# Kernel tuning notes

Measured on AMD Instinct MI355X. Metric: run time of the kernel, lower is better.

Reference implementation:

```python
import jax, jax.numpy as jnp
import numpy as np

N = 10000      # nodes
E = 160000     # edges
D = 512        # hidden = input channels (residual requires equality)
OUT = 128      # output channels
G = 64         # graphs in batch


def setup_inputs() -> dict:
    key = jax.random.key(0)
    ks = jax.random.split(key, 16)
    s = 1.0 / np.sqrt(D)
    inp = {
        "x": jax.random.normal(ks[0], (N, D), jnp.float32) * 0.1,
        "edge_index": jax.random.randint(ks[1], (2, E), 0, N, dtype=jnp.int64),
        "batch": jnp.sort(jax.random.randint(ks[2], (N,), 0, G, dtype=jnp.int64)),
    }
    for i in range(5):
        inp[f"Wr{i+1}"] = jax.random.uniform(ks[3 + 2 * i], (D, D), jnp.float32, -s, s)  # lin_rel weight
        inp[f"Ws{i+1}"] = jax.random.uniform(ks[4 + 2 * i], (D, D), jnp.float32, -s, s)  # lin_root weight (no bias)
        inp[f"b{i+1}"] = jnp.zeros((D,), jnp.float32)                                     # lin_rel bias
    inp["Wlin"] = jax.random.uniform(ks[13], (D, OUT), jnp.float32, -s, s)
    inp["blin"] = jnp.zeros((OUT,), jnp.float32)
    return inp


def graph_conv(x, src, dst, Wr, Ws, b):
    # PyG GraphConv(aggr='add'): out = lin_rel(sum_{j in N(i)} x_j) + lin_root(x_i)
    agg = jax.ops.segment_sum(x[src], dst, num_segments=N)  # [N, D] scatter-add
    return agg @ Wr + b + x @ Ws


def reference(x, Wr1, Ws1, b1, Wr2, Ws2, b2, Wr3, Ws3, b3, Wr4, Ws4, b4, Wr5, Ws5, b5, Wlin, blin, edge_index, batch):
    src, dst = edge_index[0], edge_index[1]
    x = jax.nn.relu(x + graph_conv(x, src, dst, Wr1, Ws1, b1))
    x = jax.nn.relu(x + graph_conv(x, src, dst, Wr2, Ws2, b2))
    x = jax.nn.relu(x + graph_conv(x, src, dst, Wr3, Ws3, b3))
    x = jax.nn.relu(x + graph_conv(x, src, dst, Wr4, Ws4, b4))
    x = x + graph_conv(x, src, dst, Wr5, Ws5, b5)  # no relu after conv5
    # global_mean_pool over graph ids
    sums = jax.ops.segment_sum(x, batch, num_segments=G)                       # [G, D]
    cnt = jax.ops.segment_sum(jnp.ones((N, 1), x.dtype), batch, num_segments=G)
    x = sums / jnp.maximum(cnt, 1.0)
    return x @ Wlin + blin  # [G, OUT]
```

## Files before the change

### kernel.cpp

```cpp
#include <hip/hip_runtime.h>
#include <hip/hip_bf16.h>

#define NN 10000
#define EE 160000
#define DD 512
#define GG 64
#define OUTC 128
#define NBLK 628

typedef __attribute__((ext_vector_type(8))) short bf16x8;
typedef __attribute__((ext_vector_type(4))) float f32x4;

static __device__ __forceinline__ unsigned short f2bf(float f) {
  unsigned u = __builtin_bit_cast(unsigned, f);
  unsigned rounding = 0x7fffu + ((u >> 16) & 1u);
  u += rounding;
  return (unsigned short)(u >> 16);
}

static __device__ __forceinline__ void gload_lds16(const void* g, void* l) {
  __builtin_amdgcn_global_load_lds(
      (const __attribute__((address_space(1))) unsigned*)g,
      (__attribute__((address_space(3))) unsigned*)l, 16, 0, 0);
}

struct WPtrs { const float* p[10]; };

__global__ __launch_bounds__(256) void prep_all(
    WPtrs wp, unsigned short* __restrict__ WT,
    const float* __restrict__ x_in, unsigned short* __restrict__ m0,
    const int* __restrict__ batch, int* __restrict__ gstart,
    const int* __restrict__ dstv, int* __restrict__ deg) {
  int bid = blockIdx.x;
  int tid = threadIdx.x;
  if (bid < 2560) {
    __shared__ float tile[32][33];
    int z = bid >> 8;
    int rem = bid & 255;
    int by = (rem >> 4) * 32, bx = (rem & 15) * 32;
    const float* W = wp.p[z];
    unsigned short* dst = WT + (size_t)(z >> 1) * DD * 1024 + (size_t)(z & 1) * DD;
    int tx = tid & 31, ty = tid >> 5;
    for (int i = ty; i < 32; i += 8)
      tile[i][tx] = W[(size_t)(by + i) * DD + bx + tx];
    __syncthreads();
    int addI = z & 1;
    for (int i = ty; i < 32; i += 8) {
      float v = tile[tx][i];
      if (addI && (by + tx) == (bx + i)) v += 1.0f;
      dst[(size_t)(bx + i) * 1024 + by + tx] = f2bf(v);
    }
  } else if (bid < 12560) {
    int i = (bid - 2560) * 256 + tid;
    if (i < NN * DD / 2) {
      float2 v = ((const float2*)x_in)[i];
      unsigned u = (unsigned)f2bf(v.x) | ((unsigned)f2bf(v.y) << 16);
      int e = i << 1;
      int row = e >> 9, col = e & 511;
      ((unsigned*)m0)[row * 512 + 256 + (col >> 1)] = u;
    }
  } else if (bid < 12600) {
    int i = (bid - 12560) * 256 + tid;
    if (i < NN) {
      int cur = batch[i];
      int prev = (i == 0) ? -1 : batch[i - 1];
      for (int g = prev + 1; g <= cur; ++g) gstart[g] = i;
      if (i == NN - 1)
        for (int g = cur + 1; g <= GG; ++g) gstart[g] = NN;
    }
  } else {
    int e = (bid - 12600) * 256 + tid;
    if (e < EE) atomicAdd(&deg[dstv[e]], 1);
  }
}

__global__ void scan_offsets(const int* __restrict__ cnt, int* __restrict__ offs) {
  __shared__ int wpre[17];
  __shared__ int carry;
  int t = threadIdx.x;
  int lane = t & 63, wv = t >> 6;
  if (t == 0) carry = 0;
  __syncthreads();
  for (int base = 0; base < NN; base += 1024) {
    int i = base + t;
    int v = (i < NN) ? cnt[i] : 0;
    int s = v;
#pragma unroll
    for (int d = 1; d < 64; d <<= 1) {
      int o = __shfl_up(s, d, 64);
      if (lane >= d) s += o;
    }
    if (lane == 63) wpre[wv] = s;
    __syncthreads();
    if (t == 0) {
      int r = 0;
      for (int w = 0; w < 16; ++w) { int x = wpre[w]; wpre[w] = r; r += x; }
      wpre[16] = r;
    }
    __syncthreads();
    int incl = s + wpre[wv] + carry;
    if (i < NN) offs[i] = incl - v;
    __syncthreads();
    if (t == 0) carry += wpre[16];
    __syncthreads();
  }
  if (t == 0) offs[NN] = carry;
}

__global__ void fill_edges(const int* __restrict__ src, const int* __restrict__ dst,
                           const int* __restrict__ offs, int* __restrict__ fptr,
                           int* __restrict__ ssrc) {
  int e = blockIdx.x * 256 + threadIdx.x;
  if (e < EE) {
    int d = dst[e];
    int p = atomicAdd(&fptr[d], 1);
    ssrc[offs[d] + p] = src[e];
  }
}

__global__ __launch_bounds__(256) void seg_sum2(unsigned short* __restrict__ merged,
                                                const int* __restrict__ offs,
                                                const int* __restrict__ ssrc) {
  int bid = blockIdx.x;
  int slice = bid & 3;
  int p = bid >> 2;
  int wave = threadIdx.x >> 6, lane = threadIdx.x & 63;
  int na = p * 4 + wave;
  int nb = na + 5000;
  const unsigned* xw = (const unsigned*)merged;
  size_t co = 256 + slice * 64 + lane;
  int e0 = offs[na], f0 = offs[na + 1];
  int e1 = offs[nb], f1 = offs[nb + 1];
  float a0 = 0.f, a1 = 0.f, b0 = 0.f, b1 = 0.f;
#define LD(n, ee, i) unsigned n = xw[(size_t)ssrc[(ee) + (i)] * 512 + co]
#define AC(n, x0, x1)                                   \
  x0 += __builtin_bit_cast(float, n << 16);             \
  x1 += __builtin_bit_cast(float, n & 0xffff0000u)
  while (e0 + 8 <= f0 && e1 + 8 <= f1) {
    LD(u0, e0, 0); LD(u1, e0, 1); LD(u2, e0, 2); LD(u3, e0, 3);
    LD(u4, e0, 4); LD(u5, e0, 5); LD(u6, e0, 6); LD(u7, e0, 7);
    LD(w0, e1, 0); LD(w1, e1, 1); LD(w2, e1, 2); LD(w3, e1, 3);
    LD(w4, e1, 4); LD(w5, e1, 5); LD(w6, e1, 6); LD(w7, e1, 7);
    AC(u0, a0, a1); AC(u1, a0, a1); AC(u2, a0, a1); AC(u3, a0, a1);
    AC(u4, a0, a1); AC(u5, a0, a1); AC(u6, a0, a1); AC(u7, a0, a1);
    AC(w0, b0, b1); AC(w1, b0, b1); AC(w2, b0, b1); AC(w3, b0, b1);
    AC(w4, b0, b1); AC(w5, b0, b1); AC(w6, b0, b1); AC(w7, b0, b1);
    e0 += 8; e1 += 8;
  }
  for (; e0 + 4 <= f0; e0 += 4) {
    LD(u0, e0, 0); LD(u1, e0, 1); LD(u2, e0, 2); LD(u3, e0, 3);
    AC(u0, a0, a1); AC(u1, a0, a1); AC(u2, a0, a1); AC(u3, a0, a1);
  }
  for (; e0 < f0; ++e0) {
    LD(u0, e0, 0); AC(u0, a0, a1);
  }
  for (; e1 + 4 <= f1; e1 += 4) {
    LD(w0, e1, 0); LD(w1, e1, 1); LD(w2, e1, 2); LD(w3, e1, 3);
    AC(w0, b0, b1); AC(w1, b0, b1); AC(w2, b0, b1); AC(w3, b0, b1);
  }
  for (; e1 < f1; ++e1) {
    LD(w0, e1, 0); AC(w0, b0, b1);
  }
#undef LD
#undef AC
  unsigned oa = (unsigned)f2bf(a0) | ((unsigned)f2bf(a1) << 16);
  unsigned ob = (unsigned)f2bf(b0) | ((unsigned)f2bf(b1) << 16);
  ((unsigned*)merged)[(size_t)na * 512 + slice * 64 + lane] = oa;
  ((unsigned*)merged)[(size_t)nb * 512 + slice * 64 + lane] = ob;
}

__global__ __launch_bounds__(256) void gemm_layer(
    const unsigned short* __restrict__ Am,
    const unsigned short* __restrict__ Bw,
    const float* __restrict__ bias,
    unsigned short* __restrict__ xout,
    int do_relu) {
  __shared__ unsigned short Al[2][64 * 64];
  __shared__ unsigned short Bl[2][128 * 64];
  int tid = threadIdx.x;
  int lane = tid & 63, wave = tid >> 6;
  int wr = wave >> 1, wc = wave & 1;

  int orig = blockIdx.x;
  int xcd = orig & 7, cidx = orig >> 3;
  int wgid = (xcd < 4) ? xcd * 79 + cidx : 316 + (xcd - 4) * 78 + cidx;
  int brow = (wgid >> 2) * 64;
  int bcol = (wgid & 3) * 128;
  int lrow = lane & 15, lq = lane >> 4;

  f32x4 acc[2][4];
#pragma unroll
  for (int m = 0; m < 2; ++m)
#pragma unroll
    for (int n = 0; n < 4; ++n) acc[m][n] = (f32x4){0.f, 0.f, 0.f, 0.f};

  auto STAGE = [&](int buf, int t) {
    int k0 = t * 64;
#pragma unroll
    for (int i = 0; i < 2; ++i) {
      int idx = i * 256 + tid;
      int row = idx >> 3, c = idx & 7;
      int csw = (c ^ (row & 7)) * 8;
      int gr = brow + row;
      if (gr >= NN) gr = NN - 1;
      gload_lds16(Am + (size_t)gr * 1024 + k0 + csw, &Al[buf][idx * 8]);
    }
#pragma unroll
    for (int i = 0; i < 4; ++i) {
      int idx = i * 256 + tid;
      int row = idx >> 3, c = idx & 7;
      int csw = (c ^ (row & 7)) * 8;
      gload_lds16(Bw + (size_t)(bcol + row) * 1024 + k0 + csw, &Bl[buf][idx * 8]);
    }
  };

  STAGE(0, 0);
  __syncthreads();
  int cur = 0;
#pragma unroll 1
  for (int t = 0; t < 16; ++t) {
    if (t < 15) STAGE(cur ^ 1, t + 1);
#pragma unroll
    for (int kk = 0; kk < 2; ++kk) {
      bf16x8 a[2], b[4];
      int lc = kk * 4 + lq;
#pragma unroll
      for (int m = 0; m < 2; ++m) {
        int row = wr * 32 + m * 16 + lrow;
        a[m] = *(const bf16x8*)&Al[cur][row * 64 + ((lc ^ (lrow & 7)) * 8)];
      }
#pragma unroll
      for (int n = 0; n < 4; ++n) {
        int row = wc * 64 + n * 16 + lrow;
        b[n] = *(const bf16x8*)&Bl[cur][row * 64 + ((lc ^ (lrow & 7)) * 8)];
      }
#pragma unroll
      for (int m = 0; m < 2; ++m)
#pragma unroll
        for (int n = 0; n < 4; ++n)
          acc[m][n] = __builtin_amdgcn_mfma_f32_16x16x32_bf16(a[m], b[n], acc[m][n], 0, 0, 0);
    }
    __syncthreads();
    cur ^= 1;
  }

  int crow = lq * 4, ccol = lrow;
#pragma unroll
  for (int m = 0; m < 2; ++m) {
#pragma unroll
    for (int n = 0; n < 4; ++n) {
      int col = bcol + wc * 64 + n * 16 + ccol;
      float bv = bias[col];
#pragma unroll
      for (int i = 0; i < 4; ++i) {
        int row = brow + wr * 32 + m * 16 + crow + i;
        if (row < NN) {
          float v = acc[m][n][i] + bv;
          if (do_relu) v = fmaxf(v, 0.f);
          xout[(size_t)row * 1024 + 512 + col] = f2bf(v);
        }
      }
    }
  }
}

__global__ __launch_bounds__(256) void pool_partial(const unsigned short* __restrict__ mfin,
                                                    const int* __restrict__ gstart,
                                                    float* __restrict__ pooled) {
  int g = blockIdx.x, part = blockIdx.y;
  int t = threadIdx.x;
  int beg = gstart[g], end = gstart[g + 1];
  int n = end - beg;
  int per = (n + 7) >> 3;
  int b = beg + part * per;
  int e = b + per; if (e > end) e = end;
  if (b >= e) return;
  const unsigned* mw = (const unsigned*)mfin;
  float a0 = 0.f, a1 = 0.f;
  for (int r = b; r < e; ++r) {
    unsigned v = mw[(size_t)r * 512 + 256 + t];
    a0 += __builtin_bit_cast(float, v << 16);
    a1 += __builtin_bit_cast(float, v & 0xffff0000u);
  }
  atomicAdd(&pooled[g * DD + 2 * t], a0);
  atomicAdd(&pooled[g * DD + 2 * t + 1], a1);
}

__global__ __launch_bounds__(128) void final_linear(const float* __restrict__ pooled,
                                                    const int* __restrict__ gstart,
                                                    const float* __restrict__ Wlin,
                                                    const float* __restrict__ blin,
                                                    float* __restrict__ out) {
  __shared__ float p[128];
  int g = blockIdx.x, kq = blockIdx.y;
  int o = threadIdx.x;
  int cnt = gstart[g + 1] - gstart[g];
  float inv = 1.0f / fmaxf((float)cnt, 1.0f);
  p[o] = pooled[g * DD + kq * 128 + o] * inv;
  __syncthreads();
  float s = (kq == 0) ? blin[o] : 0.f;
#pragma unroll 8
  for (int k = 0; k < 128; ++k)
    s += p[k] * Wlin[(size_t)(kq * 128 + k) * OUTC + o];
  atomicAdd(&out[g * OUTC + o], s);
}

extern "C" void kernel_launch(void* const* d_in, const int* in_sizes, int n_in,
                              void* d_out, int out_size, void* d_ws, size_t ws_size,
                              hipStream_t stream) {
  const float* x_in = (const float*)d_in[0];
  const int* ei = (const int*)d_in[1];
  const int* src = ei;
  const int* dst = ei + EE;
  const int* batch = (const int*)d_in[2];
  WPtrs wp;
  const float* bias[5];
  for (int l = 0; l < 5; ++l) {
    wp.p[2 * l] = (const float*)d_in[3 + 3 * l];
    wp.p[2 * l + 1] = (const float*)d_in[4 + 3 * l];
    bias[l] = (const float*)d_in[5 + 3 * l];
  }
  const float* Wlin = (const float*)d_in[18];
  const float* blin = (const float*)d_in[19];
  float* out = (float*)d_out;

  char* ws = (char*)d_ws;
  size_t off = 0;
  auto alloc = [&](size_t bytes) { size_t o = off; off += (bytes + 511) & ~(size_t)511; return o; };
  unsigned short* m0 = (unsigned short*)(ws + alloc((size_t)NN * 1024 * 2));
  unsigned short* m1 = (unsigned short*)(ws + alloc((size_t)NN * 1024 * 2));
  unsigned short* wt = (unsigned short*)(ws + alloc((size_t)5 * DD * 1024 * 2));
  int* deg = (int*)(ws + alloc((size_t)2 * NN * 4));
  int* fptr = deg + NN;
  int* offs = (int*)(ws + alloc((size_t)(NN + 1) * 4));
  int* ssrc = (int*)(ws + alloc((size_t)EE * 4));
  int* gstart = (int*)(ws + alloc((size_t)(GG + 1) * 4));
  float* pooled = (float*)(ws + alloc((size_t)GG * DD * 4));

  hipMemsetAsync(deg, 0, (size_t)2 * NN * 4, stream);
  hipMemsetAsync(pooled, 0, (size_t)GG * DD * 4, stream);
  hipMemsetAsync(out, 0, (size_t)GG * OUTC * 4, stream);

  prep_all<<<13225, 256, 0, stream>>>(wp, wt, x_in, m0, batch, gstart, dst, deg);

  scan_offsets<<<1, 1024, 0, stream>>>(deg, offs);
  fill_edges<<<(EE + 255) / 256, 256, 0, stream>>>(src, dst, offs, fptr, ssrc);

  unsigned short* mc = m0;
  unsigned short* mn = m1;
  for (int l = 0; l < 5; ++l) {
    seg_sum2<<<5000, 256, 0, stream>>>(mc, offs, ssrc);
    gemm_layer<<<NBLK, 256, 0, stream>>>(mc, wt + (size_t)l * DD * 1024,
                                         bias[l], mn, l < 4 ? 1 : 0);
    unsigned short* t = mc; mc = mn; mn = t;
  }

  dim3 pgrid(GG, 8);
  pool_partial<<<pgrid, 256, 0, stream>>>(mc, gstart, pooled);
  dim3 fgrid(GG, 4);
  final_linear<<<fgrid, 128, 0, stream>>>(pooled, gstart, Wlin, blin, out);
}
```

Baseline: 258.9 us.

## Steal segment-sum work per XCD and fuse pooling with final linear

The segment-sum kernel now has each block claim its work item from per-slice atomic counters, choosing first the slice that matches its XCD id. The aim is for the same XCD to keep gathering the same 64-column feature slice so it stays in that XCD's L2. Separately, pool_partial and final_linear are merged into one kernel per graph that computes the mean, does the 512x128 matvec, and writes the output directly. This removes the pooled buffer, two memsets and the float atomics. The cost is one atomic per block and less parallelism in the pooling step (64 blocks instead of 512).

```diff
diff --git a/kernel.cpp b/kernel.cpp
--- a/kernel.cpp
+++ b/kernel.cpp
@@ -118,13 +118,29 @@
   }
 }
 
-__global__ __launch_bounds__(256) void seg_sum2(unsigned short* __restrict__ merged,
-                                                const int* __restrict__ offs,
-                                                const int* __restrict__ ssrc) {
-  int bid = blockIdx.x;
-  int slice = bid & 3;
-  int p = bid >> 2;
-  int wave = threadIdx.x >> 6, lane = threadIdx.x & 63;
+__global__ __launch_bounds__(256) void seg_steal(unsigned short* __restrict__ merged,
+                                                 const int* __restrict__ offs,
+                                                 const int* __restrict__ ssrc,
+                                                 int* __restrict__ ctr) {
+  __shared__ int sel;
+  int tid = threadIdx.x;
+  if (tid == 0) {
+    unsigned xcd = __builtin_amdgcn_s_getreg(20 | (31 << 11));
+    int item = -1;
+#pragma unroll
+    for (int k = 0; k < 4; ++k) {
+      if (item < 0) {
+        int s = (int)((xcd + k) & 3u);
+        int g = atomicAdd(&ctr[s], 1);
+        if (g < 1250) item = s * 1250 + g;
+      }
+    }
+    sel = item;
+  }
+  __syncthreads();
+  int slice = sel / 1250;
+  int p = sel - slice * 1250;
+  int wave = tid >> 6, lane = tid & 63;
   int na = p * 4 + wave;
   int nb = na + 5000;
   const unsigned* xw = (const unsigned*)merged;
@@ -264,45 +280,51 @@
   }
 }
 
-__global__ __launch_bounds__(256) void pool_partial(const unsigned short* __restrict__ mfin,
-                                                    const int* __restrict__ gstart,
-                                                    float* __restrict__ pooled) {
-  int g = blockIdx.x, part = blockIdx.y;
+__global__ __launch_bounds__(256) void pool_final(const unsigned short* __restrict__ mfin,
+                                                  const int* __restrict__ gstart,
+                                                  const float* __restrict__ Wlin,
+                                                  const float* __restrict__ blin,
+                                                  float* __restrict__ out) {
+  __shared__ float pl[DD];
+  __shared__ float red[OUTC];
+  int g = blockIdx.x;
   int t = threadIdx.x;
   int beg = gstart[g], end = gstart[g + 1];
-  int n = end - beg;
-  int per = (n + 7) >> 3;
-  int b = beg + part * per;
-  int e = b + per; if (e > end) e = end;
-  if (b >= e) return;
   const unsigned* mw = (const unsigned*)mfin;
   float a0 = 0.f, a1 = 0.f;
-  for (int r = b; r < e; ++r) {
+  int r = beg;
+  for (; r + 4 <= end; r += 4) {
+    unsigned v0 = mw[(size_t)r * 512 + 256 + t];
+    unsigned v1 = mw[(size_t)(r + 1) * 512 + 256 + t];
+    unsigned v2 = mw[(size_t)(r + 2) * 512 + 256 + t];
+    unsigned v3 = mw[(size_t)(r + 3) * 512 + 256 + t];
+    a0 += __builtin_bit_cast(float, v0 << 16);
+    a1 += __builtin_bit_cast(float, v0 & 0xffff0000u);
+    a0 += __builtin_bit_cast(float, v1 << 16);
+    a1 += __builtin_bit_cast(float, v1 & 0xffff0000u);
+    a0 += __builtin_bit_cast(float, v2 << 16);
+    a1 += __builtin_bit_cast(float, v2 & 0xffff0000u);
+    a0 += __builtin_bit_cast(float, v3 << 16);
+    a1 += __builtin_bit_cast(float, v3 & 0xffff0000u);
+  }
+  for (; r < end; ++r) {
     unsigned v = mw[(size_t)r * 512 + 256 + t];
     a0 += __builtin_bit_cast(float, v << 16);
     a1 += __builtin_bit_cast(float, v & 0xffff0000u);
   }
-  atomicAdd(&pooled[g * DD + 2 * t], a0);
-  atomicAdd(&pooled[g * DD + 2 * t + 1], a1);
-}
-
-__global__ __launch_bounds__(128) void final_linear(const float* __restrict__ pooled,
-                                                    const int* __restrict__ gstart,
-                                                    const float* __restrict__ Wlin,
-                                                    const float* __restrict__ blin,
-                                                    float* __restrict__ out) {
-  __shared__ float p[128];
-  int g = blockIdx.x, kq = blockIdx.y;
-  int o = threadIdx.x;
-  int cnt = gstart[g + 1] - gstart[g];
-  float inv = 1.0f / fmaxf((float)cnt, 1.0f);
-  p[o] = pooled[g * DD + kq * 128 + o] * inv;
-  __syncthreads();
-  float s = (kq == 0) ? blin[o] : 0.f;
+  float inv = 1.0f / fmaxf((float)(end - beg), 1.0f);
+  pl[2 * t] = a0 * inv;
+  pl[2 * t + 1] = a1 * inv;
+  __syncthreads();
+  int o = t & 127, h = t >> 7;
+  float s = 0.f;
+  int kb = h * 256;
 #pragma unroll 8
-  for (int k = 0; k < 128; ++k)
-    s += p[k] * Wlin[(size_t)(kq * 128 + k) * OUTC + o];
-  atomicAdd(&out[g * OUTC + o], s);
+  for (int k = 0; k < 256; ++k)
+    s += pl[kb + k] * Wlin[(size_t)(kb + k) * OUTC + o];
+  if (h == 1) red[o] = s;
+  __syncthreads();
+  if (h == 0) out[g * OUTC + o] = s + red[o] + blin[o];
 }
 
 extern "C" void kernel_launch(void* const* d_in, const int* in_sizes, int n_in,
@@ -330,16 +352,14 @@
   unsigned short* m0 = (unsigned short*)(ws + alloc((size_t)NN * 1024 * 2));
   unsigned short* m1 = (unsigned short*)(ws + alloc((size_t)NN * 1024 * 2));
   unsigned short* wt = (unsigned short*)(ws + alloc((size_t)5 * DD * 1024 * 2));
-  int* deg = (int*)(ws + alloc((size_t)2 * NN * 4));
+  int* deg = (int*)(ws + alloc((size_t)(2 * NN + 32) * 4));
   int* fptr = deg + NN;
+  int* ctr = deg + 2 * NN;
   int* offs = (int*)(ws + alloc((size_t)(NN + 1) * 4));
   int* ssrc = (int*)(ws + alloc((size_t)EE * 4));
   int* gstart = (int*)(ws + alloc((size_t)(GG + 1) * 4));
-  float* pooled = (float*)(ws + alloc((size_t)GG * DD * 4));
-
-  hipMemsetAsync(deg, 0, (size_t)2 * NN * 4, stream);
-  hipMemsetAsync(pooled, 0, (size_t)GG * DD * 4, stream);
-  hipMemsetAsync(out, 0, (size_t)GG * OUTC * 4, stream);
+
+  hipMemsetAsync(deg, 0, (size_t)(2 * NN + 32) * 4, stream);
 
   prep_all<<<13225, 256, 0, stream>>>(wp, wt, x_in, m0, batch, gstart, dst, deg);
 
@@ -349,14 +369,11 @@
   unsigned short* mc = m0;
   unsigned short* mn = m1;
   for (int l = 0; l < 5; ++l) {
-    seg_sum2<<<5000, 256, 0, stream>>>(mc, offs, ssrc);
+    seg_steal<<<5000, 256, 0, stream>>>(mc, offs, ssrc, ctr + l * 4);
     gemm_layer<<<NBLK, 256, 0, stream>>>(mc, wt + (size_t)l * DD * 1024,
                                          bias[l], mn, l < 4 ? 1 : 0);
     unsigned short* t = mc; mc = mn; mn = t;
   }
 
-  dim3 pgrid(GG, 8);
-  pool_partial<<<pgrid, 256, 0, stream>>>(mc, gstart, pooled);
-  dim3 fgrid(GG, 4);
-  final_linear<<<fgrid, 128, 0, stream>>>(pooled, gstart, Wlin, blin, out);
-}
+  pool_final<<<GG, 256, 0, stream>>>(mc, gstart, Wlin, blin, out);
+}
```

Measured after the change: 496.5 us. +91.8%, slower.
